# Kernel optimization log

Hardware: AMD Instinct MI355X
Metric: run time of the kernel (lower is better)

The kernel has to match this reference:

```python
import jax, jax.numpy as jnp
import numpy as np

B = 1024      # batch
DIN = 103     # generator/encoder input dim
L1, L2 = 64, 32   # encoder layer widths (latent = 32)
E = 8         # NUM_EXPERTS
GH = 64       # gating hidden width
H = 256       # generator hidden width
DOUT = 51     # generator output dim
EPS = 1e-5    # BatchNorm eps


def setup_inputs() -> dict:
    key = jax.random.key(0)
    ks = jax.random.split(key, 24)
    s = 0.05
    f32 = jnp.float32
    return {
        "x": jax.random.normal(ks[0], (B, DIN), f32),
        # encoder Linear + BN params
        "w1": jax.random.normal(ks[1], (L1, DIN), f32) * s,
        "b1": jnp.zeros((L1,), f32),
        "gamma1": jnp.ones((L1,), f32),
        "beta1": jnp.zeros((L1,), f32),
        "w2": jax.random.normal(ks[2], (L2, L1), f32) * s,
        "b2": jnp.zeros((L2,), f32),
        "gamma2": jnp.ones((L2,), f32),
        "beta2": jnp.zeros((L2,), f32),
        # gating MLP (latent 32 -> GH -> GH -> E, ELU, softmax)
        "gw1": jax.random.normal(ks[3], (GH, L2), f32) * s,
        "gb1": jnp.zeros((GH,), f32),
        "gw2": jax.random.normal(ks[4], (GH, GH), f32) * s,
        "gb2": jnp.zeros((GH,), f32),
        "gw3": jax.random.normal(ks[5], (E, GH), f32) * s,
        "gb3": jnp.zeros((E,), f32),
        # expert weight banks for 3-layer generator (MANN style)
        "ew1": jax.random.normal(ks[6], (E, DIN, H), f32) * s,
        "eb1": jnp.zeros((E, H), f32),
        "ew2": jax.random.normal(ks[7], (E, H, H), f32) * s,
        "eb2": jnp.zeros((E, H), f32),
        "ew3": jax.random.normal(ks[8], (E, H, DOUT), f32) * s,
        "eb3": jnp.zeros((E, DOUT), f32),
    }


def _batchnorm(h, gamma, beta):
    # training-mode BatchNorm1d: per-batch mean/var (biased var, matching torch)
    m = jnp.mean(h, axis=0)
    v = jnp.mean((h - m) ** 2, axis=0)
    return gamma * (h - m) * jax.lax.rsqrt(v + EPS) + beta


def reference(x, w1, b1, gamma1, beta1, w2, b2, gamma2, beta2,
              gw1, gb1, gw2, gb2, gw3, gb3,
              ew1, eb1, ew2, eb2, ew3, eb3):
    # in-place scale of last 3 features (x[:,100:103] *= 100)
    xs = x.at[:, 100:103].multiply(100.0)
    # encoder: Linear -> BN -> ReLU, twice
    h = jax.nn.relu(_batchnorm(xs @ w1.T + b1, gamma1, beta1))
    latent = jax.nn.relu(_batchnorm(h @ w2.T + b2, gamma2, beta2))
    # gating network -> blending coefficients BC [B, E]
    g = jax.nn.elu(latent @ gw1.T + gb1)
    g = jax.nn.elu(g @ gw2.T + gb2)
    bc = jax.nn.softmax(g @ gw3.T + gb3, axis=-1)
    # MANN-style generator: per-sample expert-blended weights
    wb1 = jnp.einsum('be,eih->bih', bc, ew1)   # [B, DIN, H]
    h1 = jax.nn.elu(jnp.einsum('bi,bih->bh', xs, wb1) + bc @ eb1)
    wb2 = jnp.einsum('be,ehk->bhk', bc, ew2)   # [B, H, H]
    h2 = jax.nn.elu(jnp.einsum('bh,bhk->bk', h1, wb2) + bc @ eb2)
    wb3 = jnp.einsum('be,eho->bho', bc, ew3)   # [B, H, DOUT]
    out = jnp.einsum('bh,bho->bo', h2, wb3) + bc @ eb3
    return out
```

## Files before the change

kernel.cpp:

```cpp
#include <hip/hip_runtime.h>
#include <math.h>


#define DIN 103
#define NE  8
#define HH  256
#define DOUT 51
#define EPSBN 1e-5f

typedef __attribute__((ext_vector_type(8))) short bf16x8;
typedef __attribute__((ext_vector_type(4))) float f32x4;
typedef __attribute__((ext_vector_type(8))) unsigned short us8;
typedef unsigned short ushort_t;

__device__ __forceinline__ float eluf(float v) { return v > 0.f ? v : (expf(v) - 1.f); }
__device__ __forceinline__ unsigned short bf16h(float f) {
  unsigned u = __float_as_uint(f);
  u += 0x7FFFu + ((u >> 16) & 1u);
  return (unsigned short)(u >> 16);
}
__device__ __forceinline__ float bf16f(unsigned short h) { return __uint_as_float(((unsigned)h) << 16); }
__device__ __forceinline__ void split_bf16(float v, unsigned short& h, unsigned short& l) {
  h = bf16h(v);
  l = bf16h(v - bf16f(h));
}
#define MFMA __builtin_amdgcn_mfma_f32_16x16x32_bf16

__device__ __forceinline__ void stA(float* p, float v) {
  __hip_atomic_store(p, v, __ATOMIC_RELAXED, __HIP_MEMORY_SCOPE_AGENT);
}
__device__ __forceinline__ float ldA(const float* p) {
  return __hip_atomic_load((float*)p, __ATOMIC_RELAXED, __HIP_MEMORY_SCOPE_AGENT);
}
__device__ __forceinline__ void stAu(unsigned* p, unsigned v) {
  __hip_atomic_store(p, v, __ATOMIC_RELAXED, __HIP_MEMORY_SCOPE_AGENT);
}
__device__ __forceinline__ unsigned ldAu(const unsigned* p) {
  return __hip_atomic_load((unsigned*)p, __ATOMIC_RELAXED, __HIP_MEMORY_SCOPE_AGENT);
}
union U16B { us8 v; bf16x8 b; unsigned u[4]; };
__device__ __forceinline__ void st16A(void* p, us8 x) {
  U16B t; t.v = x;
  unsigned* d = (unsigned*)p;
#pragma unroll
  for (int j = 0; j < 4; ++j) stAu(d + j, t.u[j]);
}
__device__ __forceinline__ bf16x8 ld16A(const void* p) {
  U16B t;
  const unsigned* s = (const unsigned*)p;
#pragma unroll
  for (int j = 0; j < 4; ++j) t.u[j] = ldAu(s + j);
  return t.b;
}

#define O_SLOTS1 0
#define O_SLOTS2 8192
#define O_H1RAW  20480
#define O_H2RAW  86016
#define O_XSH    118784
#define O_XSL    184320
#define O_E1H    258048
#define O_E1L    389120
#define O_E2H    520192
#define O_E3H    782336
#define O_A1H    847872
#define O_A1L    978944
#define O_A2H    1110016
#define O_A2L    1241088
#define O_BAR    1372160

__device__ __forceinline__ void gbar(unsigned* c) {
  asm volatile("s_waitcnt vmcnt(0)" ::: "memory");
  __syncthreads();
  if (threadIdx.x == 0) {
    __hip_atomic_fetch_add(c, 1u, __ATOMIC_RELAXED, __HIP_MEMORY_SCOPE_AGENT);
    while (__hip_atomic_load(c, __ATOMIC_RELAXED, __HIP_MEMORY_SCOPE_AGENT) < 256u)
      __builtin_amdgcn_s_sleep(2);
  }
  __syncthreads();
}

__global__ __launch_bounds__(256) void k_prep_enc1(
    const float* __restrict__ x, const float* __restrict__ w1, const float* __restrict__ b1,
    const float* __restrict__ ew1, const float* __restrict__ ew2, const float* __restrict__ ew3,
    float* __restrict__ ws) {
  __shared__ union {
    float tile[32][65];
    float xt[16][104];
    struct { float w1L[64 * DIN]; float xr[16][104]; float hb[16][64]; } e1;
  } sm;
  int bk = blockIdx.x, t = threadIdx.x;
  int l2 = t & 63, c = l2 & 15, q = l2 >> 4;
  if (bk == 0 && t < 4) ((unsigned*)(ws + O_BAR))[t] = 0u;

  if (bk < 256) {
    int nh = bk & 3, kc = (bk >> 2) & 7, e = bk >> 5;
    int k0 = kc * 32, n0 = nh * 64;
#pragma unroll
    for (int i = 0; i < 8; ++i) {
      int kl = (t >> 6) + i * 4;
      sm.tile[kl][t & 63] = ew2[((size_t)e * HH + k0 + kl) * HH + n0 + (t & 63)];
    }
    __syncthreads();
    int nsl = t >> 6;
    us8 H8;
#pragma unroll
    for (int j = 0; j < 8; ++j) H8[j] = bf16h(sm.tile[q * 8 + j][nsl * 16 + c]);
    size_t dst = (((size_t)(e * 16 + nh * 4 + nsl)) * 8 + kc) * 512 + l2 * 8;
    *(us8*)((ushort_t*)(ws + O_E2H) + dst) = H8;
  } else if (bk < 384) {
    int b2 = bk - 256;
    int nh = b2 & 3, kc = (b2 >> 2) & 3, e = b2 >> 4;
    int k0 = kc * 32, n0 = nh * 64;
#pragma unroll
    for (int i = 0; i < 8; ++i) {
      int kl = (t >> 6) + i * 4;
      int k = k0 + kl;
      sm.tile[kl][t & 63] = (k < DIN) ? ew1[((size_t)e * DIN + k) * HH + n0 + (t & 63)] : 0.f;
    }
    __syncthreads();
    int nsl = t >> 6;
    us8 H8, L8;
#pragma unroll
    for (int j = 0; j < 8; ++j) {
      unsigned short h, lo; split_bf16(sm.tile[q * 8 + j][nsl * 16 + c], h, lo);
      H8[j] = h; L8[j] = lo;
    }
    size_t dst = (((size_t)(e * 16 + nh * 4 + nsl)) * 4 + kc) * 512 + l2 * 8;
    *(us8*)((ushort_t*)(ws + O_E1H) + dst) = H8;
    *(us8*)((ushort_t*)(ws + O_E1L) + dst) = L8;
  } else if (bk < 448) {
    int b2 = bk - 384;
    int kc = b2 & 7, e = b2 >> 3;
    int k0 = kc * 32;
#pragma unroll
    for (int i = 0; i < 8; ++i) {
      int kl = (t >> 6) + i * 4;
      int n = t & 63;
      sm.tile[kl][n] = (n < DOUT) ? ew3[((size_t)e * HH + k0 + kl) * DOUT + n] : 0.f;
    }
    __syncthreads();
    int nsl = t >> 6;
    us8 H8;
#pragma unroll
    for (int j = 0; j < 8; ++j) H8[j] = bf16h(sm.tile[q * 8 + j][nsl * 16 + c]);
    size_t dst = (((size_t)(e * 4 + nsl)) * 8 + kc) * 512 + l2 * 8;
    *(us8*)((ushort_t*)(ws + O_E3H) + dst) = H8;
  } else if (bk < 512) {
    int msub = bk - 448;
    for (int i = t; i < 16 * 104; i += 256) {
      int b = i / 104, k = i - b * 104;
      float v = 0.f;
      if (k < DIN) { v = x[(size_t)(msub * 16 + b) * DIN + k]; if (k >= 100) v *= 100.f; }
      sm.xt[b][k] = v;
    }
    __syncthreads();
    int kc = t >> 6;
    int m = c;
    us8 H8, L8;
#pragma unroll
    for (int j = 0; j < 8; ++j) {
      int k = kc * 32 + q * 8 + j;
      float v = (k < 104) ? sm.xt[m][k] : 0.f;
      unsigned short h, lo; split_bf16(v, h, lo);
      H8[j] = h; L8[j] = lo;
    }
    size_t dst = ((size_t)msub * 4 + kc) * 512 + l2 * 8;
    *(us8*)((ushort_t*)(ws + O_XSH) + dst) = H8;
    *(us8*)((ushort_t*)(ws + O_XSL) + dst) = L8;
  } else {
    float* slots1 = ws + O_SLOTS1;
    float* h1raw  = ws + O_H1RAW;
    int bkl = bk - 512;
    int r0 = bkl * 16;
    for (int i = t; i < 64 * DIN; i += 256) sm.e1.w1L[i] = w1[i];
    for (int i = t; i < 16 * 104; i += 256) {
      int r = i / 104, c2 = i - r * 104;
      float v = 0.f;
      if (c2 < DIN) { v = x[(size_t)(r0 + r) * DIN + c2]; if (c2 >= 100) v *= 100.f; }
      sm.e1.xr[r][c2] = v;
    }
    __syncthreads();
#pragma unroll
    for (int i = 0; i < 4; ++i) {
      int idx = t + i * 256;
      int r = idx >> 6, j = idx & 63;
      float acc = b1[j];
      for (int k = 0; k < DIN; ++k) acc = fmaf(sm.e1.xr[r][k], sm.e1.w1L[j * DIN + k], acc);
      sm.e1.hb[r][j] = acc;
      h1raw[(size_t)(r0 + r) * 64 + j] = acc;
    }
    __syncthreads();
    if (t < 64) {
      float s = 0.f, qq = 0.f;
      for (int r = 0; r < 16; ++r) { float v = sm.e1.hb[r][t]; s += v; qq += v * v; }
      slots1[bkl * 128 + t] = s;
      slots1[bkl * 128 + 64 + t] = qq;
    }
  }
}

__global__ __launch_bounds__(256) void k_rest(
    const float* __restrict__ gamma1, const float* __restrict__ beta1,
    const float* __restrict__ w2, const float* __restrict__ b2,
    const float* __restrict__ gamma2, const float* __restrict__ beta2,
    const float* __restrict__ gw1, const float* __restrict__ gb1,
    const float* __restrict__ gw2, const float* __restrict__ gb2,
    const float* __restrict__ gw3, const float* __restrict__ gb3,
    const float* __restrict__ eb1, const float* __restrict__ eb2,
    const float* __restrict__ eb3,
    float* __restrict__ ws, float* __restrict__ out) {
  __shared__ union {
    struct { float w2T[64 * 33]; float red[128]; float sc1[64], sh1[64];
             float h1b[16][64]; float hb2[16][32]; } enc2;
    struct { float gw1L[64 * 33]; float gw2L[64 * 65]; float gw3L[8 * 65];
             float gb1L[64], gb2L[64], gb3L[8];
             float red2[64], sc2[32], sh2[32];
             float lat[16][32]; float g1[16][64], g2[16][64]; } gate;
    struct { float hT[64][17]; float ebs[512]; } comb;
    struct { float p3s[8][16][64]; float eb3L[8][64]; } g3;
  } U;
  __shared__ float bcL[16][8];

  const int blk = blockIdx.x, t = threadIdx.x;
  const int m = blk >> 2, g = blk & 3;
  const int wv = t >> 6, l = t & 63, c = l & 15, quad = l >> 4;
  const int R0 = m * 16;
  unsigned* bar = (unsigned*)(ws + O_BAR);
  const ushort_t* XsH = (const ushort_t*)(ws + O_XSH);
  const ushort_t* XsL = (const ushort_t*)(ws + O_XSL);
  const ushort_t* E1H = (const ushort_t*)(ws + O_E1H);
  const ushort_t* E1L = (const ushort_t*)(ws + O_E1L);
  const ushort_t* E2H = (const ushort_t*)(ws + O_E2H);
  const ushort_t* E3H = (const ushort_t*)(ws + O_E3H);

  bf16x8 a1h[4], a1l[4];
#pragma unroll
  for (int kc = 0; kc < 4; ++kc) {
    a1h[kc] = *(const bf16x8*)(XsH + ((size_t)m * 4 + kc) * 512 + l * 8);
    a1l[kc] = *(const bf16x8*)(XsL + ((size_t)m * 4 + kc) * 512 + l * 8);
  }

  if (blk < 64) {
    float* slots1 = ws + O_SLOTS1;
    float* slots2 = ws + O_SLOTS2;
    float* h1raw  = ws + O_H1RAW;
    float* h2raw  = ws + O_H2RAW;
    const int R0e = blk * 16;
    for (int i = t; i < 2048; i += 256) { int j = i >> 6, k = i & 63; U.enc2.w2T[k * 33 + j] = w2[i]; }
    if (t < 128) {
      float s = 0.f;
      for (int b = 0; b < 64; ++b) s += slots1[b * 128 + t];
      U.enc2.red[t] = s;
    }
    __syncthreads();
    if (t < 64) {
      float mm = U.enc2.red[t] * (1.f / 1024.f);
      float v = U.enc2.red[64 + t] * (1.f / 1024.f) - mm * mm;
      float sc = gamma1[t] * rsqrtf(v + EPSBN);
      U.enc2.sc1[t] = sc; U.enc2.sh1[t] = beta1[t] - mm * sc;
    }
    __syncthreads();
#pragma unroll
    for (int i = 0; i < 4; ++i) {
      int idx = t + i * 256;
      int r = idx >> 6, k = idx & 63;
      U.enc2.h1b[r][k] = fmaxf(fmaf(h1raw[(size_t)(R0e + r) * 64 + k], U.enc2.sc1[k], U.enc2.sh1[k]), 0.f);
    }
    __syncthreads();
#pragma unroll
    for (int i = 0; i < 2; ++i) {
      int o = t + i * 256;
      int r = o >> 5, j = o & 31;
      float acc = b2[j];
      for (int k = 0; k < 64; ++k) acc = fmaf(U.enc2.h1b[r][k], U.enc2.w2T[k * 33 + j], acc);
      U.enc2.hb2[r][j] = acc;
      stA(h2raw + (size_t)(R0e + r) * 32 + j, acc);
    }
    __syncthreads();
    if (t < 32) {
      float s = 0.f, q = 0.f;
      for (int r = 0; r < 16; ++r) { float v = U.enc2.hb2[r][t]; s += v; q += v * v; }
      stA(slots2 + blk * 64 + t, s);
      stA(slots2 + blk * 64 + 32 + t, q);
    }
  } else {
    for (int i = t; i < 2048; i += 256) { int j = i >> 5, k = i & 31; U.gate.gw1L[j * 33 + k] = gw1[i]; }
    for (int i = t; i < 4096; i += 256) { int j = i >> 6, k = i & 63; U.gate.gw2L[j * 65 + k] = gw2[i]; }
    for (int i = t; i < 512; i += 256) { int j = i >> 6, k = i & 63; U.gate.gw3L[j * 65 + k] = gw3[i]; }
    if (t < 64) { U.gate.gb1L[t] = gb1[t]; U.gate.gb2L[t] = gb2[t]; }
    if (t < 8) U.gate.gb3L[t] = gb3[t];
  }
  gbar(bar + 0);

  {
    const float* slots2 = ws + O_SLOTS2;
    const float* h2raw  = ws + O_H2RAW;
    if (blk < 64) {
      for (int i = t; i < 2048; i += 256) { int j = i >> 5, k = i & 31; U.gate.gw1L[j * 33 + k] = gw1[i]; }
      for (int i = t; i < 4096; i += 256) { int j = i >> 6, k = i & 63; U.gate.gw2L[j * 65 + k] = gw2[i]; }
      for (int i = t; i < 512; i += 256) { int j = i >> 6, k = i & 63; U.gate.gw3L[j * 65 + k] = gw3[i]; }
      if (t < 64) { U.gate.gb1L[t] = gb1[t]; U.gate.gb2L[t] = gb2[t]; }
      if (t < 8) U.gate.gb3L[t] = gb3[t];
    }
    if (t < 64) {
      float vvv[64];
#pragma unroll
      for (int b = 0; b < 64; ++b) vvv[b] = ldA(slots2 + b * 64 + t);
      float s = 0.f;
#pragma unroll
      for (int b = 0; b < 64; ++b) s += vvv[b];
      U.gate.red2[t] = s;
    }
    __syncthreads();
    if (t < 32) {
      float mm = U.gate.red2[t] * (1.f / 1024.f);
      float v = U.gate.red2[32 + t] * (1.f / 1024.f) - mm * mm;
      float sc = gamma2[t] * rsqrtf(v + EPSBN);
      U.gate.sc2[t] = sc; U.gate.sh2[t] = beta2[t] - mm * sc;
    }
    __syncthreads();
#pragma unroll
    for (int i = 0; i < 2; ++i) {
      int idx = t + i * 256;
      int r = idx >> 5, cc = idx & 31;
      U.gate.lat[r][cc] = fmaxf(fmaf(ldA(h2raw + (size_t)(R0 + r) * 32 + cc), U.gate.sc2[cc], U.gate.sh2[cc]), 0.f);
    }
    __syncthreads();
#pragma unroll
    for (int rr = 0; rr < 4; ++rr) {
      int r = wv * 4 + rr;
      float a1 = U.gate.gb1L[l];
      for (int k = 0; k < 32; ++k) a1 = fmaf(U.gate.gw1L[l * 33 + k], U.gate.lat[r][k], a1);
      U.gate.g1[r][l] = eluf(a1);
    }
    __syncthreads();
#pragma unroll
    for (int rr = 0; rr < 4; ++rr) {
      int r = wv * 4 + rr;
      float a2 = U.gate.gb2L[l];
      for (int k = 0; k < 64; ++k) a2 = fmaf(U.gate.gw2L[l * 65 + k], U.gate.g1[r][k], a2);
      U.gate.g2[r][l] = eluf(a2);
    }
    __syncthreads();
#pragma unroll
    for (int rr = 0; rr < 4; ++rr) {
      int r = wv * 4 + rr;
      if (l < 8) {
        float a3 = U.gate.gb3L[l];
        for (int k = 0; k < 64; ++k) a3 = fmaf(U.gate.gw3L[l * 65 + k], U.gate.g2[r][k], a3);
        float mx = a3;
        mx = fmaxf(mx, __shfl_xor(mx, 1));
        mx = fmaxf(mx, __shfl_xor(mx, 2));
        mx = fmaxf(mx, __shfl_xor(mx, 4));
        float p = expf(a3 - mx);
        float sp = p;
        sp += __shfl_xor(sp, 1); sp += __shfl_xor(sp, 2); sp += __shfl_xor(sp, 4);
        bcL[r][l] = p / sp;
      }
    }
    __syncthreads();

    for (int i = t; i < 512; i += 256) U.comb.ebs[i] = eb1[(i >> 6) * HH + g * 64 + (i & 63)];
    __syncthreads();
    const int ns = g * 4 + wv;
    f32x4 blend = {};
#pragma unroll
    for (int e = 0; e < NE; ++e) {
      float bcv[4];
#pragma unroll
      for (int r = 0; r < 4; ++r) bcv[r] = bcL[quad * 4 + r][e];
      f32x4 acc = {};
#pragma unroll
      for (int kc = 0; kc < 4; ++kc) {
        size_t bo = (((size_t)(e * 16 + ns)) * 4 + kc) * 512 + l * 8;
        bf16x8 bh = *(const bf16x8*)(E1H + bo);
        bf16x8 bl = *(const bf16x8*)(E1L + bo);
        acc = MFMA(a1h[kc], bh, acc, 0, 0, 0);
        acc = MFMA(a1l[kc], bh, acc, 0, 0, 0);
        acc = MFMA(a1h[kc], bl, acc, 0, 0, 0);
      }
      float ebv = U.comb.ebs[e * 64 + wv * 16 + c];
#pragma unroll
      for (int r = 0; r < 4; ++r) blend[r] = fmaf(bcv[r], acc[r] + ebv, blend[r]);
    }
#pragma unroll
    for (int r = 0; r < 4; ++r) U.comb.hT[wv * 16 + c][quad * 4 + r] = eluf(blend[r]);
    __syncthreads();
    if (t < 128) {
      int kcl = t >> 6, l2 = t & 63, row = l2 & 15, k0l = kcl * 32 + (l2 >> 4) * 8;
      us8 H, L;
#pragma unroll
      for (int j = 0; j < 8; ++j) {
        unsigned short h, lo; split_bf16(U.comb.hT[k0l + j][row], h, lo);
        H[j] = h; L[j] = lo;
      }
      size_t dst = ((size_t)m * 8 + g * 2 + kcl) * 512 + l2 * 8;
      st16A((ushort_t*)(ws + O_A1H) + dst, H);
      st16A((ushort_t*)(ws + O_A1L) + dst, L);
    }
  }
  gbar(bar + 1);

  {
    const ushort_t* A1H = (const ushort_t*)(ws + O_A1H);
    const ushort_t* A1L = (const ushort_t*)(ws + O_A1L);
    for (int i = t; i < 512; i += 256) U.comb.ebs[i] = eb2[(i >> 6) * HH + g * 64 + (i & 63)];
    bf16x8 ah[8], al[8];
#pragma unroll
    for (int kc = 0; kc < 8; ++kc) {
      ah[kc] = ld16A(A1H + ((size_t)m * 8 + kc) * 512 + l * 8);
      al[kc] = ld16A(A1L + ((size_t)m * 8 + kc) * 512 + l * 8);
    }
    __syncthreads();
    const int ns = g * 4 + wv;
    f32x4 blend = {};
#pragma unroll
    for (int e = 0; e < NE; ++e) {
      float bcv[4];
#pragma unroll
      for (int r = 0; r < 4; ++r) bcv[r] = bcL[quad * 4 + r][e];
      f32x4 acc = {};
#pragma unroll
      for (int kc = 0; kc < 8; ++kc) {
        size_t bo = (((size_t)(e * 16 + ns)) * 8 + kc) * 512 + l * 8;
        bf16x8 bh = *(const bf16x8*)(E2H + bo);
        acc = MFMA(ah[kc], bh, acc, 0, 0, 0);
        acc = MFMA(al[kc], bh, acc, 0, 0, 0);
      }
      float ebv = U.comb.ebs[e * 64 + wv * 16 + c];
#pragma unroll
      for (int r = 0; r < 4; ++r) blend[r] = fmaf(bcv[r], acc[r] + ebv, blend[r]);
    }
#pragma unroll
    for (int r = 0; r < 4; ++r) U.comb.hT[wv * 16 + c][quad * 4 + r] = eluf(blend[r]);
    __syncthreads();
    if (t < 128) {
      int kcl = t >> 6, l2 = t & 63, row = l2 & 15, k0l = kcl * 32 + (l2 >> 4) * 8;
      us8 H, L;
#pragma unroll
      for (int j = 0; j < 8; ++j) {
        unsigned short h, lo; split_bf16(U.comb.hT[k0l + j][row], h, lo);
        H[j] = h; L[j] = lo;
      }
      size_t dst = ((size_t)m * 8 + g * 2 + kcl) * 512 + l2 * 8;
      st16A((ushort_t*)(ws + O_A2H) + dst, H);
      st16A((ushort_t*)(ws + O_A2L) + dst, L);
    }
  }
  gbar(bar + 2);

  if (g == 0) {
    const ushort_t* A2H = (const ushort_t*)(ws + O_A2H);
    const ushort_t* A2L = (const ushort_t*)(ws + O_A2L);
    for (int i = t; i < 512; i += 256) {
      int e2 = i >> 6, n = i & 63;
      U.g3.eb3L[e2][n] = (n < DOUT) ? eb3[e2 * DOUT + n] : 0.f;
    }
    bf16x8 ah[8], al[8];
#pragma unroll
    for (int kc = 0; kc < 8; ++kc) {
      ah[kc] = ld16A(A2H + ((size_t)m * 8 + kc) * 512 + l * 8);
      al[kc] = ld16A(A2L + ((size_t)m * 8 + kc) * 512 + l * 8);
    }
#pragma unroll
    for (int ee = 0; ee < 2; ++ee) {
      const int e = wv + ee * 4;
      f32x4 acc[4] = {};
#pragma unroll
      for (int kc = 0; kc < 8; ++kc) {
#pragma unroll
        for (int nsi = 0; nsi < 4; ++nsi) {
          size_t bo = (((size_t)(e * 4 + nsi)) * 8 + kc) * 512 + l * 8;
          bf16x8 bh = *(const bf16x8*)(E3H + bo);
          acc[nsi] = MFMA(ah[kc], bh, acc[nsi], 0, 0, 0);
          acc[nsi] = MFMA(al[kc], bh, acc[nsi], 0, 0, 0);
        }
      }
#pragma unroll
      for (int nsi = 0; nsi < 4; ++nsi)
#pragma unroll
        for (int r = 0; r < 4; ++r)
          U.g3.p3s[e][quad * 4 + r][nsi * 16 + c] = acc[nsi][r];
    }
    __syncthreads();
#pragma unroll
    for (int i = 0; i < 4; ++i) {
      int idx = t + i * 256;
      int row = idx >> 6, col = idx & 63;
      float s = 0.f;
#pragma unroll
      for (int e2 = 0; e2 < 8; ++e2)
        s = fmaf(bcL[row][e2], U.g3.p3s[e2][row][col] + U.g3.eb3L[e2][col], s);
      if (col < DOUT) out[(size_t)(R0 + row) * DOUT + col] = s;
    }
  }
}

extern "C" void kernel_launch(void* const* d_in, const int* in_sizes, int n_in,
                              void* d_out, int out_size, void* d_ws, size_t ws_size,
                              hipStream_t stream) {
  const float* x      = (const float*)d_in[0];
  const float* w1     = (const float*)d_in[1];
  const float* b1     = (const float*)d_in[2];
  const float* gamma1 = (const float*)d_in[3];
  const float* beta1  = (const float*)d_in[4];
  const float* w2     = (const float*)d_in[5];
  const float* b2     = (const float*)d_in[6];
  const float* gamma2 = (const float*)d_in[7];
  const float* beta2  = (const float*)d_in[8];
  const float* gw1    = (const float*)d_in[9];
  const float* gb1    = (const float*)d_in[10];
  const float* gw2    = (const float*)d_in[11];
  const float* gb2    = (const float*)d_in[12];
  const float* gw3    = (const float*)d_in[13];
  const float* gb3    = (const float*)d_in[14];
  const float* ew1    = (const float*)d_in[15];
  const float* eb1    = (const float*)d_in[16];
  const float* ew2    = (const float*)d_in[17];
  const float* eb2    = (const float*)d_in[18];
  const float* ew3    = (const float*)d_in[19];
  const float* eb3    = (const float*)d_in[20];
  float* wsf  = (float*)d_ws;
  float* outp = (float*)d_out;

  k_prep_enc1<<<576, 256, 0, stream>>>(x, w1, b1, ew1, ew2, ew3, wsf);
  k_rest<<<256, 256, 0, stream>>>(gamma1, beta1, w2, b2, gamma2, beta2,
                                  gw1, gb1, gw2, gb2, gw3, gb3,
                                  eb1, eb2, eb3, wsf, outp);
}
```

Measured before the change: 171.0 us.

## Replace flat grid barrier with two-level hierarchical atomic barrier

Replaces the single-counter grid barrier, where 256 blocks each atomically increment and poll one address, with a tree. Blocks first arrive on one of 16 padded group counters; the last arriver in each group increments a root counter, and the final root arriver sets 8 padded release flags that blocks poll with a longer sleep. This spreads atomic and polling traffic across cache lines to cut contention. Barrier state grows to 1024 words per barrier, zeroed by three prep blocks. The slots1 reduction loop is also batched so its loads are issued before the adds.

```diff
diff --git a/kernel.cpp b/kernel.cpp
--- a/kernel.cpp
+++ b/kernel.cpp
@@ -69,13 +69,22 @@
 #define O_A2L    1241088
 #define O_BAR    1372160
 
-__device__ __forceinline__ void gbar(unsigned* c) {
+__device__ __forceinline__ void gbar(unsigned* base, int blk) {
   asm volatile("s_waitcnt vmcnt(0)" ::: "memory");
   __syncthreads();
   if (threadIdx.x == 0) {
-    __hip_atomic_fetch_add(c, 1u, __ATOMIC_RELAXED, __HIP_MEMORY_SCOPE_AGENT);
-    while (__hip_atomic_load(c, __ATOMIC_RELAXED, __HIP_MEMORY_SCOPE_AGENT) < 256u)
-      __builtin_amdgcn_s_sleep(2);
+    unsigned a = __hip_atomic_fetch_add(base + (blk >> 4) * 16, 1u,
+                                        __ATOMIC_RELAXED, __HIP_MEMORY_SCOPE_AGENT);
+    if (a == 15u) {
+      unsigned r = __hip_atomic_fetch_add(base + 256, 1u,
+                                          __ATOMIC_RELAXED, __HIP_MEMORY_SCOPE_AGENT);
+      if (r == 15u) {
+#pragma unroll
+        for (int j = 0; j < 8; ++j) stAu(base + 272 + j * 16, 1u);
+      }
+    }
+    while (ldAu(base + 272 + (blk & 7) * 16) == 0u)
+      __builtin_amdgcn_s_sleep(16);
   }
   __syncthreads();
 }
@@ -91,7 +100,11 @@
   } sm;
   int bk = blockIdx.x, t = threadIdx.x;
   int l2 = t & 63, c = l2 & 15, q = l2 >> 4;
-  if (bk == 0 && t < 4) ((unsigned*)(ws + O_BAR))[t] = 0u;
+  if (bk < 3) {
+    unsigned* bz = (unsigned*)(ws + O_BAR) + bk * 1024;
+#pragma unroll
+    for (int i = 0; i < 4; ++i) bz[t + i * 256] = 0u;
+  }
 
   if (bk < 256) {
     int nh = bk & 3, kc = (bk >> 2) & 7, e = bk >> 5;
@@ -250,7 +263,14 @@
     for (int i = t; i < 2048; i += 256) { int j = i >> 6, k = i & 63; U.enc2.w2T[k * 33 + j] = w2[i]; }
     if (t < 128) {
       float s = 0.f;
-      for (int b = 0; b < 64; ++b) s += slots1[b * 128 + t];
+#pragma unroll
+      for (int ch = 0; ch < 2; ++ch) {
+        float arr[32];
+#pragma unroll
+        for (int b = 0; b < 32; ++b) arr[b] = slots1[(ch * 32 + b) * 128 + t];
+#pragma unroll
+        for (int b = 0; b < 32; ++b) s += arr[b];
+      }
       U.enc2.red[t] = s;
     }
     __syncthreads();
@@ -291,7 +311,7 @@
     if (t < 64) { U.gate.gb1L[t] = gb1[t]; U.gate.gb2L[t] = gb2[t]; }
     if (t < 8) U.gate.gb3L[t] = gb3[t];
   }
-  gbar(bar + 0);
+  gbar(bar, blk);
 
   {
     const float* slots2 = ws + O_SLOTS2;
@@ -400,7 +420,7 @@
       st16A((ushort_t*)(ws + O_A1L) + dst, L);
     }
   }
-  gbar(bar + 1);
+  gbar(bar + 1024, blk);
 
   {
     const ushort_t* A1H = (const ushort_t*)(ws + O_A1H);
@@ -448,7 +468,7 @@
       st16A((ushort_t*)(ws + O_A2L) + dst, L);
     }
   }
-  gbar(bar + 2);
+  gbar(bar + 2048, blk);
 
   if (g == 0) {
     const ushort_t* A2H = (const ushort_t*)(ws + O_A2H);
```

After: 159.9 us. 6.5% less time.
